# Optimization experiments

Measured on AMD Instinct MI355X. Metric: run time of the kernel, lower is better.

## Reference

```python
import jax, jax.numpy as jnp
import numpy as np

B, S, D, H, DK, DV, L, DFF = 4, 512, 512, 8, 64, 64, 6, 2048
VE, VD, EMPTY = 32000, 32000, 0


def _pos_encoding(dim, seq):
    # Faithful to the repo's PositionalEncoding: angle = pos / 10000**(2*i/dim),
    # i the raw dim index (not i//2), entry (pos, 0) forced to 0, row 0 all zeros,
    # sin on even cols / cos on odd cols applied to rows 1:.
    i = np.arange(dim)
    p = np.arange(seq)[:, None].astype(np.float64)
    pe = np.where(i == 0, 0.0, p / 10000.0 ** (2.0 * i / dim))
    pe[1:, 0::2] = np.sin(pe[1:, 0::2])
    pe[1:, 1::2] = np.cos(pe[1:, 1::2])
    return jnp.asarray(pe, dtype=jnp.float32)


POS = _pos_encoding(D, S)  # [S, D]


def _ln(x, g, b):
    m = x.mean(-1, keepdims=True)
    v = ((x - m) ** 2).mean(-1, keepdims=True)
    return (x - m) / jnp.sqrt(v + 1e-6) * g + b


def _mhsa(xq, xkv, mask, Wq, Wk, Wv, Wo, g, b):
    # xq [B,Sq,D], xkv [B,Sk,D], mask [B,Sq,Sk] bool (True = masked)
    q = (xq @ Wq).reshape(xq.shape[0], xq.shape[1], H, DK)
    k = (xkv @ Wk).reshape(xkv.shape[0], xkv.shape[1], H, DK)
    v = (xkv @ Wv).reshape(xkv.shape[0], xkv.shape[1], H, DV)
    scores = jnp.einsum('bqhd,bkhd->bhqk', q, k) / jnp.sqrt(jnp.float32(DK))
    # faithful to torch.masked_fill(attn, mask, 1e-09): fill value, not -inf
    scores = jnp.where(mask[:, None, :, :], jnp.float32(1e-9), scores)
    attn = jax.nn.softmax(scores, axis=-1)
    out = jnp.einsum('bhqk,bkhd->bqhd', attn, v).reshape(xq.shape[0], xq.shape[1], H * DV)
    return _ln(out @ Wo + xq, g, b)


def _ffn(x, W1, c1, W2, c2, g, b):
    h = jax.nn.leaky_relu(x @ W1 + c1, 0.01)
    return _ln(h @ W2 + c2 + x, g, b)


def _forward(encoder_input, decoder_input, emb_enc, emb_dec, enc_params, dec_params, proj_W):
    Bsz = encoder_input.shape[0]
    enc_pad = jnp.broadcast_to((encoder_input == EMPTY)[:, None, :], (Bsz, S, S))
    sub = jnp.triu(jnp.ones((S, S), dtype=bool), 1)
    dec_mask = jnp.broadcast_to((decoder_input == EMPTY)[:, None, :], (Bsz, S, S)) | sub[None]

    x = emb_enc[encoder_input] + POS

    def enc_block(h, p):
        Wq, Wk, Wv, Wo, g1, b1, W1, c1, W2, c2, g2, b2 = p
        h = _mhsa(h, h, enc_pad, Wq, Wk, Wv, Wo, g1, b1)
        h = _ffn(h, W1, c1, W2, c2, g2, b2)
        return h, None

    enc_out, _ = jax.lax.scan(enc_block, x, enc_params)

    y = emb_dec[decoder_input] + POS

    def dec_block(h, p):
        Wq, Wk, Wv, Wo, g1, b1, W1, c1, W2, c2, g2, b2 = p
        h = _mhsa(h, h, dec_mask, Wq, Wk, Wv, Wo, g1, b1)
        # Faithful to source: TransformerDecodingLayer calls self.attention for BOTH
        # self-attention and cross-attention (same weights), with enc_out as k/v.
        h = _mhsa(h, enc_out, enc_pad, Wq, Wk, Wv, Wo, g1, b1)
        h = _ffn(h, W1, c1, W2, c2, g2, b2)
        return h, None

    dec_out, _ = jax.lax.scan(dec_block, y, dec_params)
    return dec_out @ proj_W  # [B, S, VD] logits


def setup_inputs() -> dict:
    key = jax.random.key(0)
    ks = iter(jax.random.split(key, 64))
    n = lambda shape: jax.random.normal(next(ks), shape, dtype=jnp.float32) * 0.02
    inp = {
        'encoder_input': jax.random.randint(next(ks), (B, S), 0, VE, dtype=jnp.int32),
        'decoder_input': jax.random.randint(next(ks), (B, S), 0, VD, dtype=jnp.int32),
        'emb_enc': n((VE, D)),
        'emb_dec': n((VD, D)),
        'proj_W': n((D, VD)),
    }
    for pfx in ('enc', 'dec'):
        inp[pfx + '_Wq'] = n((L, D, H * DK))
        inp[pfx + '_Wk'] = n((L, D, H * DK))
        inp[pfx + '_Wv'] = n((L, D, H * DV))
        inp[pfx + '_Wo'] = n((L, H * DV, D))
        inp[pfx + '_g1'] = jnp.ones((L, D), jnp.float32)
        inp[pfx + '_b1'] = jnp.zeros((L, D), jnp.float32)
        inp[pfx + '_W1'] = n((L, D, DFF))
        inp[pfx + '_c1'] = jnp.zeros((L, DFF), jnp.float32)
        inp[pfx + '_W2'] = n((L, DFF, D))
        inp[pfx + '_c2'] = jnp.zeros((L, D), jnp.float32)
        inp[pfx + '_g2'] = jnp.ones((L, D), jnp.float32)
        inp[pfx + '_b2'] = jnp.zeros((L, D), jnp.float32)
    return inp


def reference(encoder_input, decoder_input, emb_enc, emb_dec, proj_W,
              enc_Wq, enc_Wk, enc_Wv, enc_Wo, enc_g1, enc_b1, enc_W1, enc_c1, enc_W2, enc_c2, enc_g2, enc_b2,
              dec_Wq, dec_Wk, dec_Wv, dec_Wo, dec_g1, dec_b1, dec_W1, dec_c1, dec_W2, dec_c2, dec_g2, dec_b2):
    enc_p = (enc_Wq, enc_Wk, enc_Wv, enc_Wo, enc_g1, enc_b1, enc_W1, enc_c1, enc_W2, enc_c2, enc_g2, enc_b2)
    dec_p = (dec_Wq, dec_Wk, dec_Wv, dec_Wo, dec_g1, dec_b1, dec_W1, dec_c1, dec_W2, dec_c2, dec_g2, dec_b2)
    return _forward(encoder_input, decoder_input, emb_enc, emb_dec, enc_p, dec_p, proj_W)
```

## Files before the change

### kernel.cpp

```cpp
#include <hip/hip_runtime.h>
#include <cstdint>
#include <cstddef>


#define B_   4
#define S_   512
#define D_   512
#define H_   8
#define L_   6
#define DFF_ 2048
#define VD_  32000

typedef unsigned short u16;
typedef short  s16x8  __attribute__((ext_vector_type(8)));
typedef __bf16 bf16x8 __attribute__((ext_vector_type(8)));
typedef float  f32x4  __attribute__((ext_vector_type(4)));

__device__ __forceinline__ u16 f2b(float f) {
    __bf16 h = (__bf16)f; return __builtin_bit_cast(u16, h);
}
__device__ __forceinline__ bf16x8 ld_frag(const u16* p) {
    return __builtin_bit_cast(bf16x8, *(const s16x8*)p);
}
__device__ __forceinline__ void gload16(const u16* g, u16* l) {
    __builtin_amdgcn_global_load_lds(
        (const __attribute__((address_space(1))) unsigned int*)(const void*)g,
        (__attribute__((address_space(3))) unsigned int*)(void*)l, 16, 0, 0);
}
__device__ __forceinline__ float wsum(float x) {
#pragma unroll
    for (int m = 32; m > 0; m >>= 1) x += __shfl_xor(x, m, 64);
    return x;
}

__global__ __launch_bounds__(256) void wt_k(const float* __restrict__ in0,
                                            const float* __restrict__ in1,
                                            const float* __restrict__ in2,
                                            const float* __restrict__ in3,
                                            u16* __restrict__ out,
                                            int K, int N, int Lc)
{
    const int z = blockIdx.z;
    const int tsel = z / Lc, l = z % Lc;
    const float* in = tsel == 0 ? in0 : tsel == 1 ? in1 : tsel == 2 ? in2 : in3;
    in += (size_t)l * K * N;
    u16* o = out + (size_t)z * K * N;

    const int n0 = blockIdx.x * 64, k0 = blockIdx.y * 64;
    const int tt = threadIdx.x;
    const int n = tt & 63, kq = tt >> 6;
#pragma unroll
    for (int it = 0; it < 2; ++it) {
        int k8 = kq + it * 4;
        bf16x8 ov;
#pragma unroll
        for (int j = 0; j < 8; ++j)
            ov[j] = (__bf16)in[(size_t)(k0 + k8 * 8 + j) * N + n0 + n];
        *(s16x8*)(o + (size_t)(n0 + n) * K + k0 + k8 * 8) =
            __builtin_bit_cast(s16x8, ov);
    }
}

__global__ __launch_bounds__(256) void embed_k(const int* __restrict__ idx,
                                               const float* __restrict__ emb,
                                               float* __restrict__ out,
                                               u16* __restrict__ outb)
{
    int rs = blockIdx.x;
    int s  = rs & (S_ - 1);
    int tok = idx[rs];
#pragma unroll
    for (int i = 0; i < 2; ++i) {
        int d = threadIdx.x + i * 256;
        float e  = emb[(size_t)tok * D_ + d];
        float pe = 0.0f;
        if (s > 0 && d > 0) {
            float ang = (float)s * expf(-(float)d * 0.035977892078031968f);
            pe = (d & 1) ? cosf(ang) : sinf(ang);
        }
        float x = e + pe;
        out[(size_t)rs * D_ + d]  = x;
        outb[(size_t)rs * D_ + d] = f2b(x);
    }
}

__global__ __launch_bounds__(256) void gemm_k(
    const u16* A0, const u16* A1, const u16* A2,
    const u16* B0, const u16* B1, const u16* B2,
    const float* bias0, const float* bias1, const float* bias2,
    float* Of0, float* Of1, float* Of2,
    u16* Ob0, u16* Ob1, u16* Ob2,
    u16* T0, u16* T1, u16* T2,
    int M, int N, int K, int act)
{
    const u16* A      = blockIdx.z == 0 ? A0 : (blockIdx.z == 1 ? A1 : A2);
    const u16* Bt     = blockIdx.z == 0 ? B0 : (blockIdx.z == 1 ? B1 : B2);
    const float* bias = blockIdx.z == 0 ? bias0 : (blockIdx.z == 1 ? bias1 : bias2);
    float* Of         = blockIdx.z == 0 ? Of0 : (blockIdx.z == 1 ? Of1 : Of2);
    u16* Ob           = blockIdx.z == 0 ? Ob0 : (blockIdx.z == 1 ? Ob1 : Ob2);
    u16* Tt           = blockIdx.z == 0 ? T0 : (blockIdx.z == 1 ? T1 : T2);

    __shared__ u16 As[128 * 32];
    __shared__ u16 Bs[128 * 32];

    const int t = threadIdx.x;
    const int lane = t & 63, wave = t >> 6;
    const int q = lane >> 4, r16 = lane & 15;
    const int wm = (wave & 1) * 64, wn = (wave >> 1) * 64;

    const int nwg = gridDim.x;
    const int orig = blockIdx.x;
    const int qq = nwg >> 3, rr = nwg & 7;
    const int xcd = orig & 7, loc = orig >> 3;
    const int wg = (xcd < rr ? xcd * (qq + 1) : rr * (qq + 1) + (xcd - rr) * qq) + loc;
    const int mt = M >> 7;
    const int m0 = (wg % mt) * 128, n0 = (wg / mt) * 128;

    f32x4 acc[4][4] = {};

    for (int k0 = 0; k0 < K; k0 += 32) {
#pragma unroll
        for (int r = 0; r < 2; ++r) {
            int c = wave * 2 + r;
            gload16(A + (size_t)(m0 + c * 16 + (lane >> 2)) * K + k0 + (lane & 3) * 8,
                    As + c * 512);
        }
#pragma unroll
        for (int r = 0; r < 2; ++r) {
            int c = wave * 2 + r;
            gload16(Bt + (size_t)(n0 + c * 16 + (lane >> 2)) * K + k0 + (lane & 3) * 8,
                    Bs + c * 512);
        }
        __syncthreads();

        bf16x8 af[4], bf[4];
#pragma unroll
        for (int fm = 0; fm < 4; ++fm)
            af[fm] = ld_frag(As + (wm + fm * 16 + r16) * 32 + q * 8);
#pragma unroll
        for (int fn = 0; fn < 4; ++fn)
            bf[fn] = ld_frag(Bs + (wn + fn * 16 + r16) * 32 + q * 8);
#pragma unroll
        for (int fm = 0; fm < 4; ++fm)
#pragma unroll
            for (int fn = 0; fn < 4; ++fn)
                acc[fm][fn] = __builtin_amdgcn_mfma_f32_16x16x32_bf16(
                    af[fm], bf[fn], acc[fm][fn], 0, 0, 0);
        __syncthreads();
    }

#pragma unroll
    for (int fn = 0; fn < 4; ++fn) {
        int col = n0 + wn + fn * 16 + r16;
        float bv = bias ? bias[col] : 0.0f;
#pragma unroll
        for (int fm = 0; fm < 4; ++fm) {
            int rb = m0 + wm + fm * 16 + q * 4;
            if (Tt) {
                u16 w0 = f2b(acc[fm][fn][0] + bv), w1 = f2b(acc[fm][fn][1] + bv);
                u16 w2 = f2b(acc[fm][fn][2] + bv), w3 = f2b(acc[fm][fn][3] + bv);
                uint2 pk;
                pk.x = (unsigned)w0 | ((unsigned)w1 << 16);
                pk.y = (unsigned)w2 | ((unsigned)w3 << 16);
                *(uint2*)(Tt + (((size_t)((rb >> 9) * 8 + (col >> 6)) * 64 + (col & 63)) << 9)
                             + (rb & 511)) = pk;
            } else if (Ob) {
#pragma unroll
                for (int rg = 0; rg < 4; ++rg) {
                    float x = acc[fm][fn][rg] + bv;
                    if (act) x = x >= 0.0f ? x : 0.01f * x;
                    Ob[(size_t)(rb + rg) * N + col] = f2b(x);
                }
            } else {
#pragma unroll
                for (int rg = 0; rg < 4; ++rg) {
                    float x = acc[fm][fn][rg] + bv;
                    if (act) x = x >= 0.0f ? x : 0.01f * x;
                    Of[(size_t)(rb + rg) * N + col] = x;
                }
            }
        }
    }
}

__global__ __launch_bounds__(256) void gemm64_k(
    const u16* A, const u16* Bt, const float* bias, float* O,
    int M, int N, int K)
{
    __shared__ u16 As[64 * 32];
    __shared__ u16 Bs[64 * 32];

    const int t = threadIdx.x;
    const int lane = t & 63, wave = t >> 6;
    const int q = lane >> 4, r16 = lane & 15;
    const int wm = (wave & 1) * 32, wn = (wave >> 1) * 32;

    const int nwg = gridDim.x;
    const int orig = blockIdx.x;
    const int qq = nwg >> 3, rr = nwg & 7;
    const int xcd = orig & 7, loc = orig >> 3;
    const int wg = (xcd < rr ? xcd * (qq + 1) : rr * (qq + 1) + (xcd - rr) * qq) + loc;
    const int mt = M >> 6;
    const int m0 = (wg % mt) * 64, n0 = (wg / mt) * 64;

    f32x4 acc[2][2] = {};

    for (int k0 = 0; k0 < K; k0 += 32) {
        gload16(A + (size_t)(m0 + wave * 16 + (lane >> 2)) * K + k0 + (lane & 3) * 8,
                As + wave * 512);
        gload16(Bt + (size_t)(n0 + wave * 16 + (lane >> 2)) * K + k0 + (lane & 3) * 8,
                Bs + wave * 512);
        __syncthreads();

        bf16x8 af[2], bf[2];
#pragma unroll
        for (int fm = 0; fm < 2; ++fm)
            af[fm] = ld_frag(As + (wm + fm * 16 + r16) * 32 + q * 8);
#pragma unroll
        for (int fn = 0; fn < 2; ++fn)
            bf[fn] = ld_frag(Bs + (wn + fn * 16 + r16) * 32 + q * 8);
#pragma unroll
        for (int fm = 0; fm < 2; ++fm)
#pragma unroll
            for (int fn = 0; fn < 2; ++fn)
                acc[fm][fn] = __builtin_amdgcn_mfma_f32_16x16x32_bf16(
                    af[fm], bf[fn], acc[fm][fn], 0, 0, 0);
        __syncthreads();
    }

#pragma unroll
    for (int fn = 0; fn < 2; ++fn) {
        int col = n0 + wn + fn * 16 + r16;
        float bv = bias ? bias[col] : 0.0f;
#pragma unroll
        for (int fm = 0; fm < 2; ++fm) {
            int rb = m0 + wm + fm * 16 + q * 4;
#pragma unroll
            for (int rg = 0; rg < 4; ++rg)
                O[(size_t)(rb + rg) * N + col] = acc[fm][fn][rg] + bv;
        }
    }
}

__global__ __launch_bounds__(256) void attn_k(const u16* __restrict__ Qb,
                                              const u16* __restrict__ Kb,
                                              const u16* __restrict__ Vt,
                                              u16* __restrict__ Ob,
                                              const int* __restrict__ tok,
                                              int causal)
{
    __shared__ u16 Qs[64 * 72];
    __shared__ u16 Ks[128 * 72];
    __shared__ u16 Vs[64 * 136];
    __shared__ u16 Ps[64 * 136];
    __shared__ int tokS[128];

    const int t = threadIdx.x;
    const int lane = t & 63, wave = t >> 6;
    const int q = lane >> 4, r16 = lane & 15;
    const int m0 = blockIdx.x * 64;
    const int bh = blockIdx.y, b = bh >> 3, h = bh & 7;
    const int qi = m0 + wave * 16 + r16;
    const int* kb = tok + b * S_;

#pragma unroll
    for (int r = 0; r < 2; ++r) {
        int u = t + r * 256;
        int row = u >> 3, c8 = u & 7;
        *(uint4*)(Qs + row * 72 + c8 * 8) =
            *(const uint4*)(Qb + ((size_t)(b * S_ + m0 + row)) * D_ + h * 64 + c8 * 8);
    }

    float mrun = -3.0e38f, lrun = 0.0f;
    f32x4 o[4] = {};
    const f32x4 zer = {};

    for (int kt = 0; kt < 4; ++kt) {
        const int k0 = kt * 128;
#pragma unroll
        for (int r = 0; r < 4; ++r) {
            int u = t + r * 256;
            int row = u >> 3, c8 = u & 7;
            *(uint4*)(Ks + row * 72 + c8 * 8) =
                *(const uint4*)(Kb + ((size_t)(b * S_ + k0 + row)) * D_ + h * 64 + c8 * 8);
        }
#pragma unroll
        for (int r = 0; r < 4; ++r) {
            int u = t + r * 256;
            int d = u >> 4, c = u & 15;
            *(uint4*)(Vs + d * 136 + c * 8) =
                *(const uint4*)(Vt + ((size_t)bh * 64 + d) * S_ + k0 + c * 8);
        }
        if (t < 128) tokS[t] = kb[k0 + t];
        __syncthreads();

        bf16x8 qf0 = ld_frag(Qs + (wave * 16 + r16) * 72 + 0  + q * 8);
        bf16x8 qf1 = ld_frag(Qs + (wave * 16 + r16) * 72 + 32 + q * 8);
        f32x4 s[8];
#pragma unroll
        for (int km = 0; km < 8; ++km) {
            s[km] = zer;
            s[km] = __builtin_amdgcn_mfma_f32_16x16x32_bf16(
                ld_frag(Ks + (km * 16 + r16) * 72 + 0 + q * 8), qf0, s[km], 0, 0, 0);
            s[km] = __builtin_amdgcn_mfma_f32_16x16x32_bf16(
                ld_frag(Ks + (km * 16 + r16) * 72 + 32 + q * 8), qf1, s[km], 0, 0, 0);
        }

        float tmax = -3.0e38f;
#pragma unroll
        for (int km = 0; km < 8; ++km)
#pragma unroll
            for (int rg = 0; rg < 4; ++rg) {
                int kl = km * 16 + q * 4 + rg;
                bool msk = (tokS[kl] == 0) || (causal && (k0 + kl > qi));
                float x = msk ? 1e-9f : s[km][rg] * 0.125f;
                s[km][rg] = x;
                tmax = fmaxf(tmax, x);
            }
        tmax = fmaxf(tmax, __shfl_xor(tmax, 16, 64));
        tmax = fmaxf(tmax, __shfl_xor(tmax, 32, 64));
        float mnew = fmaxf(mrun, tmax);
        float sc = __expf(mrun - mnew);
        float tsum = 0.0f;
#pragma unroll
        for (int km = 0; km < 8; ++km)
#pragma unroll
            for (int rg = 0; rg < 4; ++rg) {
                float p = __expf(s[km][rg] - mnew);
                s[km][rg] = p;
                tsum += p;
            }
        tsum += __shfl_xor(tsum, 16, 64);
        tsum += __shfl_xor(tsum, 32, 64);
        lrun = lrun * sc + tsum;
        mrun = mnew;
#pragma unroll
        for (int fm = 0; fm < 4; ++fm)
#pragma unroll
            for (int rg = 0; rg < 4; ++rg) o[fm][rg] *= sc;

#pragma unroll
        for (int km = 0; km < 8; ++km) {
            uint2 pk;
            pk.x = (unsigned)f2b(s[km][0]) | ((unsigned)f2b(s[km][1]) << 16);
            pk.y = (unsigned)f2b(s[km][2]) | ((unsigned)f2b(s[km][3]) << 16);
            *(uint2*)(Ps + (wave * 16 + r16) * 136 + km * 16 + q * 4) = pk;
        }
        __syncthreads();

        bf16x8 pf[4];
#pragma unroll
        for (int ks = 0; ks < 4; ++ks)
            pf[ks] = ld_frag(Ps + (wave * 16 + r16) * 136 + ks * 32 + q * 8);
#pragma unroll
        for (int fm = 0; fm < 4; ++fm)
#pragma unroll
            for (int ks = 0; ks < 4; ++ks)
                o[fm] = __builtin_amdgcn_mfma_f32_16x16x32_bf16(
                    ld_frag(Vs + (fm * 16 + r16) * 136 + ks * 32 + q * 8),
                    pf[ks], o[fm], 0, 0, 0);
        __syncthreads();
    }

    float inv = 1.0f / lrun;
#pragma unroll
    for (int fm = 0; fm < 4; ++fm) {
        uint2 pk;
        pk.x = (unsigned)f2b(o[fm][0] * inv) | ((unsigned)f2b(o[fm][1] * inv) << 16);
        pk.y = (unsigned)f2b(o[fm][2] * inv) | ((unsigned)f2b(o[fm][3] * inv) << 16);
        *(uint2*)(Ob + ((size_t)(b * S_ + m0 + wave * 16 + r16)) * D_
                     + h * 64 + fm * 16 + q * 4) = pk;
    }
}

__global__ __launch_bounds__(256) void ln_k(const float* __restrict__ X32,
                                            const float* resid,
                                            const float* __restrict__ g,
                                            const float* __restrict__ be,
                                            float* out, u16* outb)
{
    const int wave = threadIdx.x >> 6, lane = threadIdx.x & 63;
    const int row = blockIdx.x * 4 + wave;
    const float* xr = X32 + (size_t)row * D_;
    const float* rr = resid + (size_t)row * D_;

    float v[8];
    float s = 0.0f;
#pragma unroll
    for (int i = 0; i < 8; ++i) {
        v[i] = xr[i * 64 + lane] + rr[i * 64 + lane];
        s += v[i];
    }
    s = wsum(s);
    float mean = s * (1.0f / D_);
    float s2 = 0.0f;
#pragma unroll
    for (int i = 0; i < 8; ++i) { float d = v[i] - mean; s2 += d * d; }
    s2 = wsum(s2);
    float inv = rsqrtf(s2 * (1.0f / D_) + 1e-6f);
#pragma unroll
    for (int i = 0; i < 8; ++i) {
        int c = i * 64 + lane;
        float y = (v[i] - mean) * inv * g[c] + be[c];
        out[(size_t)row * D_ + c]  = y;
        outb[(size_t)row * D_ + c] = f2b(y);
    }
}

extern "C" void kernel_launch(void* const* d_in, const int* in_sizes, int n_in,
                              void* d_out, int out_size, void* d_ws, size_t ws_size,
                              hipStream_t stream)
{
    (void)in_sizes; (void)n_in; (void)out_size; (void)ws_size;

    const int*   enc_in  = (const int*)d_in[0];
    const int*   dec_in  = (const int*)d_in[1];
    const float* emb_enc = (const float*)d_in[2];
    const float* emb_dec = (const float*)d_in[3];
    const float* proj_W  = (const float*)d_in[4];
    const float* Wt[2][12];
    for (int p = 0; p < 2; ++p)
        for (int j = 0; j < 12; ++j)
            Wt[p][j] = (const float*)d_in[5 + p * 12 + j];

    char* ws = (char*)d_ws;
    const size_t MB = 1024 * 1024;
    float* Xe   = (float*)(ws + 0 * MB);
    float* Xd   = (float*)(ws + 4 * MB);
    float* Fo   = (float*)(ws + 8 * MB);
    u16*   HidB = (u16*)  (ws + 12 * MB);
    u16*   Qb   = (u16*)  (ws + 20 * MB);
    u16*   Kb   = (u16*)  (ws + 22 * MB);
    u16*   Vt   = (u16*)  (ws + 24 * MB);
    u16*   AtnB = (u16*)  (ws + 26 * MB);
    u16*   Xeb  = (u16*)  (ws + 28 * MB);
    u16*   Xdb  = (u16*)  (ws + 30 * MB);

    u16* WTb = (u16*)(ws + 76 * MB);
    const size_t T66 = (size_t)6 * 512 * 512;
    u16* encAT  = WTb;
    u16* encW1T = encAT  + 4 * T66;
    u16* encW2T = encW1T + 6 * (size_t)1048576;
    u16* decAT  = encW2T + 6 * (size_t)1048576;
    u16* decW1T = decAT  + 4 * T66;
    u16* decW2T = decW1T + 6 * (size_t)1048576;
    u16* projT  = decW2T + 6 * (size_t)1048576;

    const dim3 blk(256);

    for (int p = 0; p < 2; ++p) {
        u16* aT  = p ? decAT  : encAT;
        u16* w1T = p ? decW1T : encW1T;
        u16* w2T = p ? decW2T : encW2T;
        wt_k<<<dim3(8, 8, 24), blk, 0, stream>>>(Wt[p][0], Wt[p][1], Wt[p][2], Wt[p][3],
                                                 aT, 512, 512, 6);
        wt_k<<<dim3(32, 8, 6), blk, 0, stream>>>(Wt[p][6], 0, 0, 0, w1T, 512, 2048, 6);
        wt_k<<<dim3(8, 32, 6), blk, 0, stream>>>(Wt[p][8], 0, 0, 0, w2T, 2048, 512, 6);
    }
    wt_k<<<dim3(500, 8, 1), blk, 0, stream>>>(proj_W, 0, 0, 0, projT, 512, 32000, 1);

    auto gemm = [&](const u16* A0p, const u16* A1p, const u16* A2p,
                    const u16* B0p, const u16* B1p, const u16* B2p,
                    const float* c0, const float* c1p, const float* c2p,
                    float* Of0, float* Of1, float* Of2,
                    u16* Ob0, u16* Ob1, u16* Ob2,
                    u16* T0, u16* T1, u16* T2,
                    int M, int N, int K, int nz, int act) {
        dim3 g((M / 128) * (N / 128), 1, nz);
        gemm_k<<<g, blk, 0, stream>>>(A0p, A1p, A2p, B0p, B1p, B2p, c0, c1p, c2p,
                                      Of0, Of1, Of2, Ob0, Ob1, Ob2, T0, T1, T2,
                                      M, N, K, act);
    };
    auto gemm64 = [&](const u16* A, const u16* Bp, const float* c, float* O,
                      int M, int N, int K) {
        dim3 g((M / 64) * (N / 64), 1, 1);
        gemm64_k<<<g, blk, 0, stream>>>(A, Bp, c, O, M, N, K);
    };
    auto attention = [&](const u16* XqB, const u16* XkvB, const int* mtok, int causal,
                         const u16* WqT, const u16* WkT, const u16* WvT) {
        gemm(XqB, XkvB, XkvB, WqT, WkT, WvT, 0, 0, 0,
             0, 0, 0, Qb, Kb, 0, 0, 0, Vt, 2048, 512, 512, 3, 0);
        attn_k<<<dim3(8, 32), blk, 0, stream>>>(Qb, Kb, Vt, AtnB, mtok, causal);
    };

    embed_k<<<B_ * S_, blk, 0, stream>>>(enc_in, emb_enc, Xe, Xeb);
    for (int l = 0; l < L_; ++l) {
        const u16* WqT = encAT + (size_t)(0 * 6 + l) * 262144;
        const u16* WkT = encAT + (size_t)(1 * 6 + l) * 262144;
        const u16* WvT = encAT + (size_t)(2 * 6 + l) * 262144;
        const u16* WoT = encAT + (size_t)(3 * 6 + l) * 262144;
        const u16* W1T = encW1T + (size_t)l * 1048576;
        const u16* W2T = encW2T + (size_t)l * 1048576;
        const float* g1 = Wt[0][4] + l * D_;
        const float* b1 = Wt[0][5] + l * D_;
        const float* c1 = Wt[0][7] + l * DFF_;
        const float* c2 = Wt[0][9] + l * D_;
        const float* g2 = Wt[0][10] + l * D_;
        const float* b2 = Wt[0][11] + l * D_;

        attention(Xeb, Xeb, enc_in, 0, WqT, WkT, WvT);
        gemm64(AtnB, WoT, 0, Fo, 2048, 512, 512);
        ln_k<<<dim3(512), blk, 0, stream>>>(Fo, Xe, g1, b1, Xe, Xeb);
        gemm(Xeb, 0, 0, W1T, 0, 0, c1, 0, 0,
             0, 0, 0, HidB, 0, 0, 0, 0, 0, 2048, 2048, 512, 1, 1);
        gemm64(HidB, W2T, c2, Fo, 2048, 512, 2048);
        ln_k<<<dim3(512), blk, 0, stream>>>(Fo, Xe, g2, b2, Xe, Xeb);
    }

    embed_k<<<B_ * S_, blk, 0, stream>>>(dec_in, emb_dec, Xd, Xdb);
    for (int l = 0; l < L_; ++l) {
        const u16* WqT = decAT + (size_t)(0 * 6 + l) * 262144;
        const u16* WkT = decAT + (size_t)(1 * 6 + l) * 262144;
        const u16* WvT = decAT + (size_t)(2 * 6 + l) * 262144;
        const u16* WoT = decAT + (size_t)(3 * 6 + l) * 262144;
        const u16* W1T = decW1T + (size_t)l * 1048576;
        const u16* W2T = decW2T + (size_t)l * 1048576;
        const float* g1 = Wt[1][4] + l * D_;
        const float* b1 = Wt[1][5] + l * D_;
        const float* c1 = Wt[1][7] + l * DFF_;
        const float* c2 = Wt[1][9] + l * D_;
        const float* g2 = Wt[1][10] + l * D_;
        const float* b2 = Wt[1][11] + l * D_;

        attention(Xdb, Xdb, dec_in, 1, WqT, WkT, WvT);
        gemm64(AtnB, WoT, 0, Fo, 2048, 512, 512);
        ln_k<<<dim3(512), blk, 0, stream>>>(Fo, Xd, g1, b1, Xd, Xdb);

        attention(Xdb, Xeb, enc_in, 0, WqT, WkT, WvT);
        gemm64(AtnB, WoT, 0, Fo, 2048, 512, 512);
        ln_k<<<dim3(512), blk, 0, stream>>>(Fo, Xd, g1, b1, Xd, Xdb);

        gemm(Xdb, 0, 0, W1T, 0, 0, c1, 0, 0,
             0, 0, 0, HidB, 0, 0, 0, 0, 0, 2048, 2048, 512, 1, 1);
        gemm64(HidB, W2T, c2, Fo, 2048, 512, 2048);
        ln_k<<<dim3(512), blk, 0, stream>>>(Fo, Xd, g2, b2, Xd, Xdb);
    }

    gemm(Xdb, 0, 0, projT, 0, 0, 0, 0, 0,
         (float*)d_out, 0, 0, 0, 0, 0, 0, 0, 0, 2048, VD_, 512, 1, 0);
}
```

Measured before the change: 2.250 ms.

## Split-K small GEMMs, use 64-tile GEMMs, and read attention operands from global

Moves the QKV and W1 GEMMs from 128x128 tiles to 64x64 tiles to get more workgroups. The Wo and W2 GEMMs now use a two-way split-K into two fp32 buffers, and the partials and the c2 bias are summed inside the LayerNorm kernel. The attention kernel drops its LDS staging of Q, K and V and loads MFMA fragments straight from global memory, with only a per-wave wait in place of block barriers. The aim is more parallelism on the many small GEMMs and fewer syncs in attention. The cost is extra fp32 traffic for the partial sums and uncoalesced, possibly redundant global reads in attention.

```diff
diff --git a/kernel.cpp b/kernel.cpp
--- a/kernel.cpp
+++ b/kernel.cpp
@@ -85,21 +85,9 @@
 }
 
 __global__ __launch_bounds__(256) void gemm_k(
-    const u16* A0, const u16* A1, const u16* A2,
-    const u16* B0, const u16* B1, const u16* B2,
-    const float* bias0, const float* bias1, const float* bias2,
-    float* Of0, float* Of1, float* Of2,
-    u16* Ob0, u16* Ob1, u16* Ob2,
-    u16* T0, u16* T1, u16* T2,
-    int M, int N, int K, int act)
-{
-    const u16* A      = blockIdx.z == 0 ? A0 : (blockIdx.z == 1 ? A1 : A2);
-    const u16* Bt     = blockIdx.z == 0 ? B0 : (blockIdx.z == 1 ? B1 : B2);
-    const float* bias = blockIdx.z == 0 ? bias0 : (blockIdx.z == 1 ? bias1 : bias2);
-    float* Of         = blockIdx.z == 0 ? Of0 : (blockIdx.z == 1 ? Of1 : Of2);
-    u16* Ob           = blockIdx.z == 0 ? Ob0 : (blockIdx.z == 1 ? Ob1 : Ob2);
-    u16* Tt           = blockIdx.z == 0 ? T0 : (blockIdx.z == 1 ? T1 : T2);
-
+    const u16* __restrict__ A, const u16* __restrict__ Bt,
+    float* __restrict__ Of, int M, int N, int K)
+{
     __shared__ u16 As[128 * 32];
     __shared__ u16 Bs[128 * 32];
 
@@ -152,9 +140,80 @@
 #pragma unroll
     for (int fn = 0; fn < 4; ++fn) {
         int col = n0 + wn + fn * 16 + r16;
+#pragma unroll
+        for (int fm = 0; fm < 4; ++fm) {
+            int rb = m0 + wm + fm * 16 + q * 4;
+#pragma unroll
+            for (int rg = 0; rg < 4; ++rg)
+                Of[(size_t)(rb + rg) * N + col] = acc[fm][fn][rg];
+        }
+    }
+}
+
+__global__ __launch_bounds__(256) void gemm64z_k(
+    const u16* A0, const u16* A1, const u16* A2,
+    const u16* B0, const u16* B1, const u16* B2,
+    const float* bias0, const float* bias1, const float* bias2,
+    float* Of0, float* Of1, float* Of2,
+    u16* Ob0, u16* Ob1, u16* Ob2,
+    u16* T0, u16* T1, u16* T2,
+    int M, int N, int Kred, int lda, int ldb, int act)
+{
+    const int z = blockIdx.z;
+    const u16* A      = z == 0 ? A0 : (z == 1 ? A1 : A2);
+    const u16* Bt     = z == 0 ? B0 : (z == 1 ? B1 : B2);
+    const float* bias = z == 0 ? bias0 : (z == 1 ? bias1 : bias2);
+    float* Of         = z == 0 ? Of0 : (z == 1 ? Of1 : Of2);
+    u16* Ob           = z == 0 ? Ob0 : (z == 1 ? Ob1 : Ob2);
+    u16* Tt           = z == 0 ? T0 : (z == 1 ? T1 : T2);
+
+    __shared__ u16 As[64 * 32];
+    __shared__ u16 Bs[64 * 32];
+
+    const int t = threadIdx.x;
+    const int lane = t & 63, wave = t >> 6;
+    const int q = lane >> 4, r16 = lane & 15;
+    const int wm = (wave & 1) * 32, wn = (wave >> 1) * 32;
+
+    const int nwg = gridDim.x;
+    const int orig = blockIdx.x;
+    const int qq = nwg >> 3, rr = nwg & 7;
+    const int xcd = orig & 7, loc = orig >> 3;
+    const int wg = (xcd < rr ? xcd * (qq + 1) : rr * (qq + 1) + (xcd - rr) * qq) + loc;
+    const int mt = M >> 6;
+    const int m0 = (wg % mt) * 64, n0 = (wg / mt) * 64;
+
+    f32x4 acc[2][2] = {};
+
+    for (int k0 = 0; k0 < Kred; k0 += 32) {
+        gload16(A + (size_t)(m0 + wave * 16 + (lane >> 2)) * lda + k0 + (lane & 3) * 8,
+                As + wave * 512);
+        gload16(Bt + (size_t)(n0 + wave * 16 + (lane >> 2)) * ldb + k0 + (lane & 3) * 8,
+                Bs + wave * 512);
+        __syncthreads();
+
+        bf16x8 af[2], bf[2];
+#pragma unroll
+        for (int fm = 0; fm < 2; ++fm)
+            af[fm] = ld_frag(As + (wm + fm * 16 + r16) * 32 + q * 8);
+#pragma unroll
+        for (int fn = 0; fn < 2; ++fn)
+            bf[fn] = ld_frag(Bs + (wn + fn * 16 + r16) * 32 + q * 8);
+#pragma unroll
+        for (int fm = 0; fm < 2; ++fm)
+#pragma unroll
+            for (int fn = 0; fn < 2; ++fn)
+                acc[fm][fn] = __builtin_amdgcn_mfma_f32_16x16x32_bf16(
+                    af[fm], bf[fn], acc[fm][fn], 0, 0, 0);
+        __syncthreads();
+    }
+
+#pragma unroll
+    for (int fn = 0; fn < 2; ++fn) {
+        int col = n0 + wn + fn * 16 + r16;
         float bv = bias ? bias[col] : 0.0f;
 #pragma unroll
-        for (int fm = 0; fm < 4; ++fm) {
+        for (int fm = 0; fm < 2; ++fm) {
             int rb = m0 + wm + fm * 16 + q * 4;
             if (Tt) {
                 u16 w0 = f2b(acc[fm][fn][0] + bv), w1 = f2b(acc[fm][fn][1] + bv);
@@ -173,71 +232,9 @@
                 }
             } else {
 #pragma unroll
-                for (int rg = 0; rg < 4; ++rg) {
-                    float x = acc[fm][fn][rg] + bv;
-                    if (act) x = x >= 0.0f ? x : 0.01f * x;
-                    Of[(size_t)(rb + rg) * N + col] = x;
-                }
+                for (int rg = 0; rg < 4; ++rg)
+                    Of[(size_t)(rb + rg) * N + col] = acc[fm][fn][rg] + bv;
             }
-        }
-    }
-}
-
-__global__ __launch_bounds__(256) void gemm64_k(
-    const u16* A, const u16* Bt, const float* bias, float* O,
-    int M, int N, int K)
-{
-    __shared__ u16 As[64 * 32];
-    __shared__ u16 Bs[64 * 32];
-
-    const int t = threadIdx.x;
-    const int lane = t & 63, wave = t >> 6;
-    const int q = lane >> 4, r16 = lane & 15;
-    const int wm = (wave & 1) * 32, wn = (wave >> 1) * 32;
-
-    const int nwg = gridDim.x;
-    const int orig = blockIdx.x;
-    const int qq = nwg >> 3, rr = nwg & 7;
-    const int xcd = orig & 7, loc = orig >> 3;
-    const int wg = (xcd < rr ? xcd * (qq + 1) : rr * (qq + 1) + (xcd - rr) * qq) + loc;
-    const int mt = M >> 6;
-    const int m0 = (wg % mt) * 64, n0 = (wg / mt) * 64;
-
-    f32x4 acc[2][2] = {};
-
-    for (int k0 = 0; k0 < K; k0 += 32) {
-        gload16(A + (size_t)(m0 + wave * 16 + (lane >> 2)) * K + k0 + (lane & 3) * 8,
-                As + wave * 512);
-        gload16(Bt + (size_t)(n0 + wave * 16 + (lane >> 2)) * K + k0 + (lane & 3) * 8,
-                Bs + wave * 512);
-        __syncthreads();
-
-        bf16x8 af[2], bf[2];
-#pragma unroll
-        for (int fm = 0; fm < 2; ++fm)
-            af[fm] = ld_frag(As + (wm + fm * 16 + r16) * 32 + q * 8);
-#pragma unroll
-        for (int fn = 0; fn < 2; ++fn)
-            bf[fn] = ld_frag(Bs + (wn + fn * 16 + r16) * 32 + q * 8);
-#pragma unroll
-        for (int fm = 0; fm < 2; ++fm)
-#pragma unroll
-            for (int fn = 0; fn < 2; ++fn)
-                acc[fm][fn] = __builtin_amdgcn_mfma_f32_16x16x32_bf16(
-                    af[fm], bf[fn], acc[fm][fn], 0, 0, 0);
-        __syncthreads();
-    }
-
-#pragma unroll
-    for (int fn = 0; fn < 2; ++fn) {
-        int col = n0 + wn + fn * 16 + r16;
-        float bv = bias ? bias[col] : 0.0f;
-#pragma unroll
-        for (int fm = 0; fm < 2; ++fm) {
-            int rb = m0 + wm + fm * 16 + q * 4;
-#pragma unroll
-            for (int rg = 0; rg < 4; ++rg)
-                O[(size_t)(rb + rg) * N + col] = acc[fm][fn][rg] + bv;
         }
     }
 }
@@ -249,11 +246,8 @@
                                               const int* __restrict__ tok,
                                               int causal)
 {
-    __shared__ u16 Qs[64 * 72];
-    __shared__ u16 Ks[128 * 72];
-    __shared__ u16 Vs[64 * 136];
     __shared__ u16 Ps[64 * 136];
-    __shared__ int tokS[128];
+    __shared__ int tokS[512];
 
     const int t = threadIdx.x;
     const int lane = t & 63, wave = t >> 6;
@@ -263,13 +257,16 @@
     const int qi = m0 + wave * 16 + r16;
     const int* kb = tok + b * S_;
 
-#pragma unroll
-    for (int r = 0; r < 2; ++r) {
-        int u = t + r * 256;
-        int row = u >> 3, c8 = u & 7;
-        *(uint4*)(Qs + row * 72 + c8 * 8) =
-            *(const uint4*)(Qb + ((size_t)(b * S_ + m0 + row)) * D_ + h * 64 + c8 * 8);
-    }
+    tokS[t] = kb[t];
+    tokS[t + 256] = kb[t + 256];
+    __syncthreads();
+
+    const u16* qp = Qb + ((size_t)(b * S_ + m0 + wave * 16 + r16)) * D_ + h * 64 + q * 8;
+    const bf16x8 qf0 = ld_frag(qp), qf1 = ld_frag(qp + 32);
+
+    const u16* kbase = Kb + ((size_t)b * S_) * D_ + h * 64 + q * 8;
+    const u16* vbase = Vt + ((size_t)bh * 64 + r16) * S_ + q * 8;
+    u16* prow = Ps + (wave * 16 + r16) * 136;
 
     float mrun = -3.0e38f, lrun = 0.0f;
     f32x4 o[4] = {};
@@ -277,33 +274,14 @@
 
     for (int kt = 0; kt < 4; ++kt) {
         const int k0 = kt * 128;
-#pragma unroll
-        for (int r = 0; r < 4; ++r) {
-            int u = t + r * 256;
-            int row = u >> 3, c8 = u & 7;
-            *(uint4*)(Ks + row * 72 + c8 * 8) =
-                *(const uint4*)(Kb + ((size_t)(b * S_ + k0 + row)) * D_ + h * 64 + c8 * 8);
-        }
-#pragma unroll
-        for (int r = 0; r < 4; ++r) {
-            int u = t + r * 256;
-            int d = u >> 4, c = u & 15;
-            *(uint4*)(Vs + d * 136 + c * 8) =
-                *(const uint4*)(Vt + ((size_t)bh * 64 + d) * S_ + k0 + c * 8);
-        }
-        if (t < 128) tokS[t] = kb[k0 + t];
-        __syncthreads();
-
-        bf16x8 qf0 = ld_frag(Qs + (wave * 16 + r16) * 72 + 0  + q * 8);
-        bf16x8 qf1 = ld_frag(Qs + (wave * 16 + r16) * 72 + 32 + q * 8);
+
         f32x4 s[8];
 #pragma unroll
         for (int km = 0; km < 8; ++km) {
+            const u16* kp = kbase + (size_t)(k0 + km * 16 + r16) * D_;
             s[km] = zer;
-            s[km] = __builtin_amdgcn_mfma_f32_16x16x32_bf16(
-                ld_frag(Ks + (km * 16 + r16) * 72 + 0 + q * 8), qf0, s[km], 0, 0, 0);
-            s[km] = __builtin_amdgcn_mfma_f32_16x16x32_bf16(
-                ld_frag(Ks + (km * 16 + r16) * 72 + 32 + q * 8), qf1, s[km], 0, 0, 0);
+            s[km] = __builtin_amdgcn_mfma_f32_16x16x32_bf16(ld_frag(kp), qf0, s[km], 0, 0, 0);
+            s[km] = __builtin_amdgcn_mfma_f32_16x16x32_bf16(ld_frag(kp + 32), qf1, s[km], 0, 0, 0);
         }
 
         float tmax = -3.0e38f;
@@ -312,7 +290,7 @@
 #pragma unroll
             for (int rg = 0; rg < 4; ++rg) {
                 int kl = km * 16 + q * 4 + rg;
-                bool msk = (tokS[kl] == 0) || (causal && (k0 + kl > qi));
+                bool msk = (tokS[k0 + kl] == 0) || (causal && (k0 + kl > qi));
                 float x = msk ? 1e-9f : s[km][rg] * 0.125f;
                 s[km][rg] = x;
                 tmax = fmaxf(tmax, x);
@@ -344,22 +322,22 @@
             uint2 pk;
             pk.x = (unsigned)f2b(s[km][0]) | ((unsigned)f2b(s[km][1]) << 16);
             pk.y = (unsigned)f2b(s[km][2]) | ((unsigned)f2b(s[km][3]) << 16);
-            *(uint2*)(Ps + (wave * 16 + r16) * 136 + km * 16 + q * 4) = pk;
-        }
-        __syncthreads();
+            *(uint2*)(prow + km * 16 + q * 4) = pk;
+        }
+        asm volatile("s_waitcnt lgkmcnt(0)" ::: "memory");
 
         bf16x8 pf[4];
 #pragma unroll
         for (int ks = 0; ks < 4; ++ks)
-            pf[ks] = ld_frag(Ps + (wave * 16 + r16) * 136 + ks * 32 + q * 8);
-#pragma unroll
-        for (int fm = 0; fm < 4; ++fm)
+            pf[ks] = ld_frag(prow + ks * 32 + q * 8);
+#pragma unroll
+        for (int fm = 0; fm < 4; ++fm) {
+            const u16* vp = vbase + (size_t)(fm * 16) * S_ + k0;
 #pragma unroll
             for (int ks = 0; ks < 4; ++ks)
                 o[fm] = __builtin_amdgcn_mfma_f32_16x16x32_bf16(
-                    ld_frag(Vs + (fm * 16 + r16) * 136 + ks * 32 + q * 8),
-                    pf[ks], o[fm], 0, 0, 0);
-        __syncthreads();
+                    ld_frag(vp + ks * 32), pf[ks], o[fm], 0, 0, 0);
+        }
     }
 
     float inv = 1.0f / lrun;
@@ -373,23 +351,28 @@
     }
 }
 
-__global__ __launch_bounds__(256) void ln_k(const float* __restrict__ X32,
-                                            const float* resid,
+__global__ __launch_bounds__(256) void ln_k(const float* __restrict__ X1,
+                                            const float* X2,
+                                            const float* __restrict__ resid,
+                                            const float* cb,
                                             const float* __restrict__ g,
                                             const float* __restrict__ be,
                                             float* out, u16* outb)
 {
     const int wave = threadIdx.x >> 6, lane = threadIdx.x & 63;
     const int row = blockIdx.x * 4 + wave;
-    const float* xr = X32 + (size_t)row * D_;
-    const float* rr = resid + (size_t)row * D_;
+    const size_t ro = (size_t)row * D_;
 
     float v[8];
     float s = 0.0f;
 #pragma unroll
     for (int i = 0; i < 8; ++i) {
-        v[i] = xr[i * 64 + lane] + rr[i * 64 + lane];
-        s += v[i];
+        int c = i * 64 + lane;
+        float x = X1[ro + c] + resid[ro + c];
+        if (X2) x += X2[ro + c];
+        if (cb) x += cb[c];
+        v[i] = x;
+        s += x;
     }
     s = wsum(s);
     float mean = s * (1.0f / D_);
@@ -402,8 +385,8 @@
     for (int i = 0; i < 8; ++i) {
         int c = i * 64 + lane;
         float y = (v[i] - mean) * inv * g[c] + be[c];
-        out[(size_t)row * D_ + c]  = y;
-        outb[(size_t)row * D_ + c] = f2b(y);
+        out[ro + c]  = y;
+        outb[ro + c] = f2b(y);
     }
 }
 
@@ -435,6 +418,7 @@
     u16*   AtnB = (u16*)  (ws + 26 * MB);
     u16*   Xeb  = (u16*)  (ws + 28 * MB);
     u16*   Xdb  = (u16*)  (ws + 30 * MB);
+    float* Fo2  = (float*)(ws + 32 * MB);
 
     u16* WTb = (u16*)(ws + 76 * MB);
     const size_t T66 = (size_t)6 * 512 * 512;
@@ -459,27 +443,39 @@
     }
     wt_k<<<dim3(500, 8, 1), blk, 0, stream>>>(proj_W, 0, 0, 0, projT, 512, 32000, 1);
 
-    auto gemm = [&](const u16* A0p, const u16* A1p, const u16* A2p,
-                    const u16* B0p, const u16* B1p, const u16* B2p,
-                    const float* c0, const float* c1p, const float* c2p,
-                    float* Of0, float* Of1, float* Of2,
-                    u16* Ob0, u16* Ob1, u16* Ob2,
-                    u16* T0, u16* T1, u16* T2,
-                    int M, int N, int K, int nz, int act) {
-        dim3 g((M / 128) * (N / 128), 1, nz);
-        gemm_k<<<g, blk, 0, stream>>>(A0p, A1p, A2p, B0p, B1p, B2p, c0, c1p, c2p,
-                                      Of0, Of1, Of2, Ob0, Ob1, Ob2, T0, T1, T2,
-                                      M, N, K, act);
+    const u16* Z = nullptr;
+    auto qkv = [&](const u16* XqB, const u16* XkvB,
+                   const u16* WqT, const u16* WkT, const u16* WvT) {
+        dim3 g((2048 / 64) * (512 / 64), 1, 3);
+        gemm64z_k<<<g, blk, 0, stream>>>(XqB, XkvB, XkvB, WqT, WkT, WvT,
+                                         0, 0, 0, 0, 0, 0,
+                                         Qb, Kb, 0, 0, 0, Vt,
+                                         2048, 512, 512, 512, 512, 0);
     };
-    auto gemm64 = [&](const u16* A, const u16* Bp, const float* c, float* O,
-                      int M, int N, int K) {
-        dim3 g((M / 64) * (N / 64), 1, 1);
-        gemm64_k<<<g, blk, 0, stream>>>(A, Bp, c, O, M, N, K);
+    auto wo = [&](const u16* WoT) {
+        dim3 g((2048 / 64) * (512 / 64), 1, 2);
+        gemm64z_k<<<g, blk, 0, stream>>>(AtnB, AtnB + 256, Z, WoT, WoT + 256, Z,
+                                         0, 0, 0, Fo, Fo2, 0,
+                                         0, 0, 0, 0, 0, 0,
+                                         2048, 512, 256, 512, 512, 0);
+    };
+    auto w1 = [&](const u16* XB, const u16* W1T, const float* c1) {
+        dim3 g((2048 / 64) * (2048 / 64), 1, 1);
+        gemm64z_k<<<g, blk, 0, stream>>>(XB, Z, Z, W1T, Z, Z,
+                                         c1, 0, 0, 0, 0, 0,
+                                         HidB, 0, 0, 0, 0, 0,
+                                         2048, 2048, 512, 512, 512, 1);
+    };
+    auto w2 = [&](const u16* W2T) {
+        dim3 g((2048 / 64) * (512 / 64), 1, 2);
+        gemm64z_k<<<g, blk, 0, stream>>>(HidB, HidB + 1024, Z, W2T, W2T + 1024, Z,
+                                         0, 0, 0, Fo, Fo2, 0,
+                                         0, 0, 0, 0, 0, 0,
+                                         2048, 512, 1024, 2048, 2048, 0);
     };
     auto attention = [&](const u16* XqB, const u16* XkvB, const int* mtok, int causal,
                          const u16* WqT, const u16* WkT, const u16* WvT) {
-        gemm(XqB, XkvB, XkvB, WqT, WkT, WvT, 0, 0, 0,
-             0, 0, 0, Qb, Kb, 0, 0, 0, Vt, 2048, 512, 512, 3, 0);
+        qkv(XqB, XkvB, WqT, WkT, WvT);
         attn_k<<<dim3(8, 32), blk, 0, stream>>>(Qb, Kb, Vt, AtnB, mtok, causal);
     };
 
@@ -499,12 +495,11 @@
         const float* b2 = Wt[0][11] + l * D_;
 
         attention(Xeb, Xeb, enc_in, 0, WqT, WkT, WvT);
-        gemm64(AtnB, WoT, 0, Fo, 2048, 512, 512);
-        ln_k<<<dim3(512), blk, 0, stream>>>(Fo, Xe, g1, b1, Xe, Xeb);
-        gemm(Xeb, 0, 0, W1T, 0, 0, c1, 0, 0,
-             0, 0, 0, HidB, 0, 0, 0, 0, 0, 2048, 2048, 512, 1, 1);
-        gemm64(HidB, W2T, c2, Fo, 2048, 512, 2048);
-        ln_k<<<dim3(512), blk, 0, stream>>>(Fo, Xe, g2, b2, Xe, Xeb);
+        wo(WoT);
+        ln_k<<<dim3(512), blk, 0, stream>>>(Fo, Fo2, Xe, 0, g1, b1, Xe, Xeb);
+        w1(Xeb, W1T, c1);
+        w2(W2T);
+        ln_k<<<dim3(512), blk, 0, stream>>>(Fo, Fo2, Xe, c2, g2, b2, Xe, Xeb);
     }
 
     embed_k<<<B_ * S_, blk, 0, stream>>>(dec_in, emb_dec, Xd, Xdb);
@@ -523,19 +518,20 @@
         const float* b2 = Wt[1][11] + l * D_;
 
         attention(Xdb, Xdb, dec_in, 1, WqT, WkT, WvT);
-        gemm64(AtnB, WoT, 0, Fo, 2048, 512, 512);
-        ln_k<<<dim3(512), blk, 0, stream>>>(Fo, Xd, g1, b1, Xd, Xdb);
+        wo(WoT);
+        ln_k<<<dim3(512), blk, 0, stream>>>(Fo, Fo2, Xd, 0, g1, b1, Xd, Xdb);
 
         attention(Xdb, Xeb, enc_in, 0, WqT, WkT, WvT);
-        gemm64(AtnB, WoT, 0, Fo, 2048, 512, 512);
-        ln_k<<<dim3(512), blk, 0, stream>>>(Fo, Xd, g1, b1, Xd, Xdb);
-
-        gemm(Xdb, 0, 0, W1T, 0, 0, c1, 0, 0,
-             0, 0, 0, HidB, 0, 0, 0, 0, 0, 2048, 2048, 512, 1, 1);
-        gemm64(HidB, W2T, c2, Fo, 2048, 512, 2048);
-        ln_k<<<dim3(512), blk, 0, stream>>>(Fo, Xd, g2, b2, Xd, Xdb);
-    }
-
-    gemm(Xdb, 0, 0, projT, 0, 0, 0, 0, 0,
-         (float*)d_out, 0, 0, 0, 0, 0, 0, 0, 0, 2048, VD_, 512, 1, 0);
-}
+        wo(WoT);
+        ln_k<<<dim3(512), blk, 0, stream>>>(Fo, Fo2, Xd, 0, g1, b1, Xd, Xdb);
+
+        w1(Xdb, W1T, c1);
+        w2(W2T);
+        ln_k<<<dim3(512), blk, 0, stream>>>(Fo, Fo2, Xd, c2, g2, b2, Xd, Xdb);
+    }
+
+    {
+        dim3 g((2048 / 128) * (VD_ / 128), 1, 1);
+        gemm_k<<<g, blk, 0, stream>>>(Xdb, projT, (float*)d_out, 2048, VD_, 512);
+    }
+}
```

New measurement: 2.057 ms. -8.6%, faster.
